# Kernel tuning notes

Measured on AMD Instinct MI355X. Metric: run time of the kernel, lower is better.

## Reference

```python
import jax, jax.numpy as jnp
import numpy as np

B, T, E, D = 8, 2048, 1024, 128


def setup_inputs() -> dict:
    key = jax.random.key(0)
    k1, k2, k3, k4 = jax.random.split(key, 4)
    x = jax.random.normal(k1, (B, T, E), dtype=jnp.float32)
    wq = jax.random.normal(k2, (E, D), dtype=jnp.float32) * (E ** -0.5)
    wk = jax.random.normal(k3, (E, D), dtype=jnp.float32) * (E ** -0.5)
    wv = jax.random.normal(k4, (E, D), dtype=jnp.float32) * (E ** -0.5)
    return {"x": x, "wq": wq, "wk": wk, "wv": wv}


def reference(x, wq, wk, wv):
    # Projections (bias-free Linear): [B,T,E] @ [E,D] -> [B,T,D]
    q = x @ wq
    k = x @ wk
    v = x @ wv
    d = k.shape[-1]
    # Faithful to source: scores / d**(-0.5) == scores * sqrt(d)
    scores = jnp.einsum('btd,bsd->bts', q, k) * (d ** 0.5)
    causal = jnp.tril(jnp.ones((x.shape[1], x.shape[1]), dtype=bool))
    scores = jnp.where(causal, scores, -jnp.inf)
    weights = jax.nn.softmax(scores, axis=-1)  # dropout omitted (eval mode)
    return jnp.einsum('bts,bsd->btd', weights, v)
```

## Files before the change

kernel.cpp:

```cpp
#include <hip/hip_runtime.h>


#define NB 8
#define NT 2048
#define NE 1024
#define ND 128

typedef unsigned short U16;
typedef unsigned int U32;
typedef __attribute__((ext_vector_type(8))) short vbf8;
typedef __attribute__((ext_vector_type(4))) float vf4;

#define EXP2F(x) __builtin_amdgcn_exp2f(x)

__device__ __forceinline__ U16 f2bf(float f) {
  U32 u = __builtin_bit_cast(U32, f);
  u += 0x7fffu + ((u >> 16) & 1u);
  return (U16)(u >> 16);
}
__device__ __forceinline__ float bf2f(U16 h) {
  U32 u = ((U32)h) << 16;
  return __builtin_bit_cast(float, u);
}
__device__ __forceinline__ void gl_lds16(const void* g, void* l) {
  __builtin_amdgcn_global_load_lds((__attribute__((address_space(1))) void*)g,
                                   (__attribute__((address_space(3))) void*)l, 16, 0, 0);
}

__global__ void wsplit_kernel(const float* __restrict__ wq, const float* __restrict__ wk,
                              const float* __restrict__ wv, U16* __restrict__ wth,
                              U16* __restrict__ wtl) {
  int id = blockIdx.x * 256 + threadIdx.x;
  if (id >= 384 * 1024) return;
  int n = id >> 10, e = id & 1023;
  float v;
  if (n < 128)      v = wq[e * 128 + n] * 16.322231701033217f;
  else if (n < 256) v = wk[e * 128 + (n - 128)];
  else              v = wv[e * 128 + (n - 256)];
  U16 h = f2bf(v);
  wth[id] = h;
  wtl[id] = f2bf(v - bf2f(h));
}

__global__ __launch_bounds__(256, 3) void qkv_kernel(
    const float* __restrict__ x, const U16* __restrict__ wth, const U16* __restrict__ wtl,
    U16* __restrict__ qfh, U16* __restrict__ qfl, U16* __restrict__ kfh,
    U16* __restrict__ kfl, U16* __restrict__ vf) {
  __shared__ __align__(16) char smem[49152];
  char* Ah = smem;
  char* Al = smem + 8192;
  char* Bh = smem + 16384;
  char* Bl = smem + 32768;

  const int tid = threadIdx.x;
  const int w = tid >> 6, lane = tid & 63;
  const int fr = lane & 15, fq = lane >> 4;
  const int m0 = blockIdx.x * 64;
  const int nt = blockIdx.y;
  const U16* bh_src = wth + nt * (128 * 1024);
  const U16* bl_src = wtl + nt * (128 * 1024);

  const vf4 vzero = {0.f, 0.f, 0.f, 0.f};
  vf4 acc[2][4];
#pragma unroll
  for (int i = 0; i < 2; ++i)
#pragma unroll
    for (int j = 0; j < 4; ++j) acc[i][j] = vzero;

  const int wm = (w >> 1) * 32, wn = (w & 1) * 64;
  const int arow = tid >> 2, ag = tid & 3;
  const float* abase = x + (size_t)(m0 + arow) * 1024 + ag * 8;

  float v0[8], v1[8];
  {
    const float* s = abase;
    ((float4*)v0)[0] = *(const float4*)(s);
    ((float4*)v0)[1] = *(const float4*)(s + 4);
    ((float4*)v1)[0] = *(const float4*)(s + 32);
    ((float4*)v1)[1] = *(const float4*)(s + 36);
  }

  for (int k0 = 0; k0 < 1024; k0 += 64) {
#pragma unroll
    for (int p = 0; p < 4; ++p) {
      const int g = p * 256 + tid;
      const int row = g >> 3, c = g & 7;
      const int sc = c ^ (row & 7);
      const int ldsb = (p * 256 + w * 64) * 16;
      gl_lds16(bh_src + row * 1024 + k0 + sc * 8, Bh + ldsb);
      if (nt < 2) gl_lds16(bl_src + row * 1024 + k0 + sc * 8, Bl + ldsb);
    }
    {
      vbf8 h0, l0, h1, l1;
#pragma unroll
      for (int i = 0; i < 8; ++i) {
        U16 a = f2bf(v0[i]);
        h0[i] = (short)a; l0[i] = (short)f2bf(v0[i] - bf2f(a));
        U16 b = f2bf(v1[i]);
        h1[i] = (short)b; l1[i] = (short)f2bf(v1[i] - bf2f(b));
      }
      const int sw = arow & 7;
      *(vbf8*)(Ah + arow * 128 + ((ag ^ sw) << 4))       = h0;
      *(vbf8*)(Ah + arow * 128 + (((ag + 4) ^ sw) << 4)) = h1;
      if (nt < 2) {
        *(vbf8*)(Al + arow * 128 + ((ag ^ sw) << 4))       = l0;
        *(vbf8*)(Al + arow * 128 + (((ag + 4) ^ sw) << 4)) = l1;
      }
    }
    __syncthreads();

    if (k0 + 64 < 1024) {
      const float* s = abase + k0 + 64;
      ((float4*)v0)[0] = *(const float4*)(s);
      ((float4*)v0)[1] = *(const float4*)(s + 4);
      ((float4*)v1)[0] = *(const float4*)(s + 32);
      ((float4*)v1)[1] = *(const float4*)(s + 36);
    }

    if (nt < 2) {
#pragma unroll
      for (int kc = 0; kc < 2; ++kc) {
        vbf8 a_h[2], a_l[2], b_h[4], b_l[4];
#pragma unroll
        for (int i = 0; i < 2; ++i) {
          const int row = wm + i * 16 + fr;
          const int off = row * 128 + (((kc * 4 + fq) ^ (row & 7)) << 4);
          a_h[i] = *(const vbf8*)(Ah + off);
          a_l[i] = *(const vbf8*)(Al + off);
        }
#pragma unroll
        for (int j = 0; j < 4; ++j) {
          const int row = wn + j * 16 + fr;
          const int off = row * 128 + (((kc * 4 + fq) ^ (row & 7)) << 4);
          b_h[j] = *(const vbf8*)(Bh + off);
          b_l[j] = *(const vbf8*)(Bl + off);
        }
#pragma unroll
        for (int i = 0; i < 2; ++i)
#pragma unroll
          for (int j = 0; j < 4; ++j) {
            acc[i][j] = __builtin_amdgcn_mfma_f32_16x16x32_bf16(a_h[i], b_h[j], acc[i][j], 0, 0, 0);
            acc[i][j] = __builtin_amdgcn_mfma_f32_16x16x32_bf16(a_h[i], b_l[j], acc[i][j], 0, 0, 0);
            acc[i][j] = __builtin_amdgcn_mfma_f32_16x16x32_bf16(a_l[i], b_h[j], acc[i][j], 0, 0, 0);
          }
      }
    } else {
#pragma unroll
      for (int kc = 0; kc < 2; ++kc) {
        vbf8 a_h[2], b_h[4];
#pragma unroll
        for (int i = 0; i < 2; ++i) {
          const int row = wm + i * 16 + fr;
          a_h[i] = *(const vbf8*)(Ah + row * 128 + (((kc * 4 + fq) ^ (row & 7)) << 4));
        }
#pragma unroll
        for (int j = 0; j < 4; ++j) {
          const int row = wn + j * 16 + fr;
          b_h[j] = *(const vbf8*)(Bh + row * 128 + (((kc * 4 + fq) ^ (row & 7)) << 4));
        }
#pragma unroll
        for (int i = 0; i < 2; ++i)
#pragma unroll
          for (int j = 0; j < 4; ++j)
            acc[i][j] = __builtin_amdgcn_mfma_f32_16x16x32_bf16(a_h[i], b_h[j], acc[i][j], 0, 0, 0);
      }
    }
    __syncthreads();
  }

  const int b = m0 >> 11;
  if (nt < 2) {
    U16* tlh = (U16*)smem;
    U16* tll = (U16*)(smem + 16896);
#pragma unroll
    for (int i = 0; i < 2; ++i)
#pragma unroll
      for (int j = 0; j < 4; ++j)
#pragma unroll
        for (int r = 0; r < 4; ++r) {
          const int ml = wm + i * 16 + fq * 4 + r;
          const int col = wn + j * 16 + fr;
          const float val = acc[i][j][r];
          const U16 h = f2bf(val);
          tlh[ml * 132 + col] = h;
          tll[ml * 132 + col] = f2bf(val - bf2f(h));
        }
    __syncthreads();
    U16* dh = (nt == 0) ? qfh : kfh;
    U16* dl = (nt == 0) ? qfl : kfl;
    const int g0 = (m0 & 2047) >> 4;
#pragma unroll
    for (int p = 0; p < 4; ++p) {
      const int idx = p * 256 + tid;
      const int gl = idx >> 8, kc = (idx >> 6) & 3, ln = idx & 63;
      const int row = gl * 16 + (ln & 15);
      const int colc = kc * 32 + (ln >> 4) * 8;
      const size_t o = (((size_t)b * 128 + g0 + gl) * 4 + kc) * 512 + ln * 8;
      *(vbf8*)(dh + o) = *(const vbf8*)(tlh + row * 132 + colc);
      *(vbf8*)(dl + o) = *(const vbf8*)(tll + row * 132 + colc);
    }
  } else {
    U16* tl = (U16*)smem;
#pragma unroll
    for (int i = 0; i < 2; ++i)
#pragma unroll
      for (int j = 0; j < 4; ++j)
#pragma unroll
        for (int r = 0; r < 4; ++r) {
          const int ml = wm + i * 16 + fq * 4 + r;
          const int col = wn + j * 16 + fr;
          tl[col * 68 + ml] = f2bf(acc[i][j][r]);
        }
    __syncthreads();
    const int sc0 = (m0 & 2047) >> 5;
#pragma unroll
    for (int p = 0; p < 4; ++p) {
      const int idx = p * 256 + tid;
      const int df = idx >> 7, sc = (idx >> 6) & 1, ln = idx & 63;
      const int d = df * 16 + (ln & 15);
      const int sl = sc * 32 + (ln >> 4) * 8;
      const size_t o = (((size_t)b * 8 + df) * 64 + (sc0 + sc)) * 512 + ln * 8;
      *(vbf8*)(vf + o) = *(const vbf8*)(tl + d * 68 + sl);
    }
  }
}

__global__ __launch_bounds__(256, 3) void flash_kernel(
    const U16* __restrict__ qfh, const U16* __restrict__ qfl,
    const U16* __restrict__ kfh, const U16* __restrict__ kfl,
    const U16* __restrict__ vf, float* __restrict__ out) {
  __shared__ __align__(16) char smem[25088];

  const int tid = threadIdx.x;
  const int w = tid >> 6, lane = tid & 63;
  const int fr = lane & 15, fq = lane >> 4;
  const int sq = w;
  const int bid = blockIdx.x;
  const int bb = bid & 7;
  const int jj = bid >> 3;
  const int g = (jj < 64) ? (127 - jj) : (jj - 64);
  const int q0g = g * 16;

  vbf8 q_h[4], q_l[4];
  {
    const U16* qb = qfh + ((size_t)bb * 128 + g) * 2048 + lane * 8;
    const U16* qlb = qfl + ((size_t)bb * 128 + g) * 2048 + lane * 8;
#pragma unroll
    for (int kc = 0; kc < 4; ++kc) {
      q_h[kc] = *(const vbf8*)(qb + kc * 512);
      q_l[kc] = *(const vbf8*)(qlb + kc * 512);
    }
  }

  const U16* khp = kfh + (size_t)bb * 262144 + (size_t)(sq * 4) * 2048 + lane * 8;
  const U16* klp = kfl + (size_t)bb * 262144 + (size_t)(sq * 4) * 2048 + lane * 8;
  const U16* vfp = vf + (size_t)bb * 262144 + (size_t)(sq * 2) * 512 + lane * 8;
  U16* pw = (U16*)(smem + w * 2304);

  const vf4 vzero = {0.f, 0.f, 0.f, 0.f};
  vf4 oacc[8];
#pragma unroll
  for (int i = 0; i < 8; ++i) oacc[i] = vzero;
  float m_r[4], l_r[4];
#pragma unroll
  for (int r = 0; r < 4; ++r) { m_r[r] = -__builtin_inff(); l_r[r] = 0.f; }

  const int lim = q0g + 15 - sq * 64;
  const int ntw = (lim >= 0) ? ((lim >> 8) + 1) : 0;

  for (int T = 0; T < ntw; ++T) {
    vf4 sacc[4] = {vzero, vzero, vzero, vzero};
    __builtin_amdgcn_s_setprio(1);
#pragma unroll
    for (int sf = 0; sf < 4; ++sf) {
#pragma unroll
      for (int kc = 0; kc < 4; ++kc) {
        const vbf8 kh_r = *(const vbf8*)(khp + sf * 2048 + kc * 512);
        const vbf8 kl_r = *(const vbf8*)(klp + sf * 2048 + kc * 512);
        sacc[sf] = __builtin_amdgcn_mfma_f32_16x16x32_bf16(q_h[kc], kh_r, sacc[sf], 0, 0, 0);
        sacc[sf] = __builtin_amdgcn_mfma_f32_16x16x32_bf16(q_h[kc], kl_r, sacc[sf], 0, 0, 0);
        sacc[sf] = __builtin_amdgcn_mfma_f32_16x16x32_bf16(q_l[kc], kh_r, sacc[sf], 0, 0, 0);
      }
    }
    __builtin_amdgcn_s_setprio(0);

    if (T == ntw - 1) {
#pragma unroll
      for (int sf = 0; sf < 4; ++sf) {
        const int s_g = T * 256 + sq * 64 + sf * 16 + fr;
#pragma unroll
        for (int r = 0; r < 4; ++r)
          if (s_g > q0g + fq * 4 + r) sacc[sf][r] = -__builtin_inff();
      }
    }

    float tmax[4];
#pragma unroll
    for (int r = 0; r < 4; ++r)
      tmax[r] = fmaxf(fmaxf(sacc[0][r], sacc[1][r]), fmaxf(sacc[2][r], sacc[3][r]));
#pragma unroll
    for (int off = 1; off < 16; off <<= 1)
#pragma unroll
      for (int r = 0; r < 4; ++r) tmax[r] = fmaxf(tmax[r], __shfl_xor(tmax[r], off, 64));

    vbf8 vreg[8][2];
#pragma unroll
    for (int df = 0; df < 8; ++df) {
      vreg[df][0] = *(const vbf8*)(vfp + df * 32768);
      vreg[df][1] = *(const vbf8*)(vfp + df * 32768 + 512);
    }

    bool need = false;
    float mne[4];
#pragma unroll
    for (int r = 0; r < 4; ++r) {
      need |= (tmax[r] > m_r[r]);
      const float mn = fmaxf(m_r[r], tmax[r]);
      mne[r] = (mn == -__builtin_inff()) ? 0.f : mn;
    }
    if (__any(need)) {
#pragma unroll
      for (int r = 0; r < 4; ++r) {
        const float alpha = EXP2F(m_r[r] - mne[r]);
        l_r[r] *= alpha;
        m_r[r] = fmaxf(m_r[r], tmax[r]);
#pragma unroll
        for (int i = 0; i < 8; ++i) oacc[i][r] *= alpha;
      }
    }

    float psum[4];
    U16 pb[4][4];
#pragma unroll
    for (int sf = 0; sf < 4; ++sf)
#pragma unroll
      for (int r = 0; r < 4; ++r) {
        const float pv = EXP2F(sacc[sf][r] - mne[r]);
        psum[r] = (sf == 0) ? pv : (psum[r] + pv);
        pb[sf][r] = f2bf(pv);
      }
#pragma unroll
    for (int off = 1; off < 16; off <<= 1)
#pragma unroll
      for (int r = 0; r < 4; ++r) psum[r] += __shfl_xor(psum[r], off, 64);
#pragma unroll
    for (int r = 0; r < 4; ++r) l_r[r] += psum[r];

#pragma unroll
    for (int sf = 0; sf < 4; ++sf)
#pragma unroll
      for (int r = 0; r < 4; ++r) pw[(fq * 4 + r) * 72 + sf * 16 + fr] = pb[sf][r];
    asm volatile("s_waitcnt lgkmcnt(0)" ::: "memory");
    const vbf8 pf0 = *(const vbf8*)(pw + fr * 72 + fq * 8);
    const vbf8 pf1 = *(const vbf8*)(pw + fr * 72 + 32 + fq * 8);

    __builtin_amdgcn_s_setprio(1);
#pragma unroll
    for (int df = 0; df < 8; ++df) {
      oacc[df] = __builtin_amdgcn_mfma_f32_16x16x32_bf16(pf0, vreg[df][0], oacc[df], 0, 0, 0);
      oacc[df] = __builtin_amdgcn_mfma_f32_16x16x32_bf16(pf1, vreg[df][1], oacc[df], 0, 0, 0);
    }
    __builtin_amdgcn_s_setprio(0);

    khp += 32768; klp += 32768; vfp += 4096;
  }

  __syncthreads();
  float* O_d = (float*)smem;
  float* m_s = (float*)(smem + 24576);
  float* l_s = (float*)(smem + 24832);
  if (sq > 0) {
#pragma unroll
    for (int i = 0; i < 8; ++i)
#pragma unroll
      for (int r = 0; r < 4; ++r)
        O_d[((sq - 1) * 16 + fq * 4 + r) * 128 + i * 16 + fr] = oacc[i][r];
  }
  if (fr == 0) {
#pragma unroll
    for (int r = 0; r < 4; ++r) {
      m_s[sq * 16 + fq * 4 + r] = m_r[r];
      l_s[sq * 16 + fq * 4 + r] = l_r[r];
    }
  }
  __syncthreads();
  if (sq == 0) {
#pragma unroll
    for (int r = 0; r < 4; ++r) {
      const int row = fq * 4 + r;
      float mv[4];
      float M = -__builtin_inff();
#pragma unroll
      for (int p = 0; p < 4; ++p) {
        mv[p] = m_s[p * 16 + row];
        M = fmaxf(M, mv[p]);
      }
      float wgt[4], denom = 0.f;
#pragma unroll
      for (int p = 0; p < 4; ++p) {
        wgt[p] = EXP2F(mv[p] - M);
        denom += wgt[p] * l_s[p * 16 + row];
      }
      const float inv = 1.f / denom;
#pragma unroll
      for (int i = 0; i < 8; ++i) {
        float o = wgt[0] * oacc[i][r];
#pragma unroll
        for (int p = 1; p < 4; ++p)
          o += wgt[p] * O_d[((p - 1) * 16 + row) * 128 + i * 16 + fr];
        out[(size_t)(bb * 2048 + q0g + row) * 128 + i * 16 + fr] = o * inv;
      }
    }
  }
}

extern "C" void kernel_launch(void* const* d_in, const int* in_sizes, int n_in, void* d_out,
                              int out_size, void* d_ws, size_t ws_size, hipStream_t stream) {
  const float* x = (const float*)d_in[0];
  const float* wq = (const float*)d_in[1];
  const float* wk = (const float*)d_in[2];
  const float* wv = (const float*)d_in[3];
  char* ws = (char*)d_ws;
  U16* wth = (U16*)(ws);
  U16* wtl = (U16*)(ws + 786432);
  U16* qfh = (U16*)(ws + 1572864);
  U16* qfl = (U16*)(ws + 5767168);
  U16* kfh = (U16*)(ws + 9961472);
  U16* kfl = (U16*)(ws + 14155776);
  U16* vfr = (U16*)(ws + 18350080);
  float* out = (float*)d_out;

  wsplit_kernel<<<dim3(1536), dim3(256), 0, stream>>>(wq, wk, wv, wth, wtl);
  qkv_kernel<<<dim3(256, 3), dim3(256), 0, stream>>>(x, wth, wtl, qfh, qfl, kfh, kfl, vfr);
  flash_kernel<<<dim3(1024), dim3(256), 0, stream>>>(qfh, qfl, kfh, kfl, vfr, out);
}
```

Before: 94.45 us.

## Split flash attention KV loop across two blocks and merge partials

Each query tile's KV iterations are split between two blocks that take alternating 256-key chunks. Each block writes an unnormalized partial output along with its row max and row sum to workspace, and a new merge kernel combines the two halves. The goal is to double the grid size and shorten the longest causal tiles, which improves load balance and occupancy. The cost is an extra kernel launch plus partial-output traffic (about 17 MB written and read back). The split path is used only when the workspace is large enough, and a guard handles rows whose max is -inf.

```diff
diff --git a/kernel.cpp b/kernel.cpp
--- a/kernel.cpp
+++ b/kernel.cpp
@@ -225,17 +225,20 @@
   }
 }
 
-__global__ __launch_bounds__(256, 3) void flash_kernel(
+template <int SPLIT>
+__global__ __launch_bounds__(256, 3) void flash_kernel_t(
     const U16* __restrict__ qfh, const U16* __restrict__ qfl,
     const U16* __restrict__ kfh, const U16* __restrict__ kfl,
-    const U16* __restrict__ vf, float* __restrict__ out) {
+    const U16* __restrict__ vf, float* __restrict__ out, float* __restrict__ part) {
   __shared__ __align__(16) char smem[25088];
 
   const int tid = threadIdx.x;
   const int w = tid >> 6, lane = tid & 63;
   const int fr = lane & 15, fq = lane >> 4;
   const int sq = w;
-  const int bid = blockIdx.x;
+  const int bid2 = blockIdx.x;
+  const int half = SPLIT ? (bid2 & 1) : 0;
+  const int bid = SPLIT ? (bid2 >> 1) : bid2;
   const int bb = bid & 7;
   const int jj = bid >> 3;
   const int g = (jj < 64) ? (127 - jj) : (jj - 64);
@@ -252,9 +255,12 @@
     }
   }
 
-  const U16* khp = kfh + (size_t)bb * 262144 + (size_t)(sq * 4) * 2048 + lane * 8;
-  const U16* klp = kfl + (size_t)bb * 262144 + (size_t)(sq * 4) * 2048 + lane * 8;
-  const U16* vfp = vf + (size_t)bb * 262144 + (size_t)(sq * 2) * 512 + lane * 8;
+  const U16* khp = kfh + (size_t)bb * 262144 + (size_t)(sq * 4) * 2048 + lane * 8
+                   + (size_t)half * 32768;
+  const U16* klp = kfl + (size_t)bb * 262144 + (size_t)(sq * 4) * 2048 + lane * 8
+                   + (size_t)half * 32768;
+  const U16* vfp = vf + (size_t)bb * 262144 + (size_t)(sq * 2) * 512 + lane * 8
+                   + (size_t)half * 4096;
   U16* pw = (U16*)(smem + w * 2304);
 
   const vf4 vzero = {0.f, 0.f, 0.f, 0.f};
@@ -267,8 +273,11 @@
 
   const int lim = q0g + 15 - sq * 64;
   const int ntw = (lim >= 0) ? ((lim >> 8) + 1) : 0;
-
-  for (int T = 0; T < ntw; ++T) {
+  const int my_n = SPLIT ? ((ntw > half) ? ((ntw - half + 1) >> 1) : 0) : ntw;
+  const int tstep = SPLIT ? 2 : 1;
+
+  for (int it = 0; it < my_n; ++it) {
+    const int T = half + it * tstep;
     vf4 sacc[4] = {vzero, vzero, vzero, vzero};
     __builtin_amdgcn_s_setprio(1);
 #pragma unroll
@@ -362,7 +371,7 @@
     }
     __builtin_amdgcn_s_setprio(0);
 
-    khp += 32768; klp += 32768; vfp += 4096;
+    khp += 32768 * tstep; klp += 32768 * tstep; vfp += 4096 * tstep;
   }
 
   __syncthreads();
@@ -385,6 +394,7 @@
   }
   __syncthreads();
   if (sq == 0) {
+    float* pO = SPLIT ? (part + ((size_t)(bb * 128 + g) * 2 + half) * 2112) : (float*)0;
 #pragma unroll
     for (int r = 0; r < 4; ++r) {
       const int row = fq * 4 + r;
@@ -395,23 +405,60 @@
         mv[p] = m_s[p * 16 + row];
         M = fmaxf(M, mv[p]);
       }
+      const float Mne = (M == -__builtin_inff()) ? 0.f : M;
       float wgt[4], denom = 0.f;
 #pragma unroll
       for (int p = 0; p < 4; ++p) {
-        wgt[p] = EXP2F(mv[p] - M);
+        wgt[p] = EXP2F(mv[p] - Mne);
         denom += wgt[p] * l_s[p * 16 + row];
       }
-      const float inv = 1.f / denom;
-#pragma unroll
-      for (int i = 0; i < 8; ++i) {
-        float o = wgt[0] * oacc[i][r];
-#pragma unroll
-        for (int p = 1; p < 4; ++p)
-          o += wgt[p] * O_d[((p - 1) * 16 + row) * 128 + i * 16 + fr];
-        out[(size_t)(bb * 2048 + q0g + row) * 128 + i * 16 + fr] = o * inv;
-      }
-    }
-  }
+      if (SPLIT) {
+#pragma unroll
+        for (int i = 0; i < 8; ++i) {
+          float o = wgt[0] * oacc[i][r];
+#pragma unroll
+          for (int p = 1; p < 4; ++p)
+            o += wgt[p] * O_d[((p - 1) * 16 + row) * 128 + i * 16 + fr];
+          pO[row * 128 + i * 16 + fr] = o;
+        }
+        if (fr == 0) {
+          pO[2048 + row] = M;
+          pO[2064 + row] = denom;
+        }
+      } else {
+        const float inv = 1.f / denom;
+#pragma unroll
+        for (int i = 0; i < 8; ++i) {
+          float o = wgt[0] * oacc[i][r];
+#pragma unroll
+          for (int p = 1; p < 4; ++p)
+            o += wgt[p] * O_d[((p - 1) * 16 + row) * 128 + i * 16 + fr];
+          out[(size_t)(bb * 2048 + q0g + row) * 128 + i * 16 + fr] = o * inv;
+        }
+      }
+    }
+  }
+}
+
+__global__ __launch_bounds__(256) void fmerge_kernel(const float* __restrict__ part,
+                                                     float* __restrict__ out) {
+  const int tid = threadIdx.x;
+  const int rg = blockIdx.x * 16 + (tid >> 4);
+  const int c8 = (tid & 15) * 8;
+  const int b = rg >> 11, rb = rg & 2047, g = rb >> 4, r16 = rb & 15;
+  const float* p0 = part + ((size_t)(b * 128 + g) * 2 + 0) * 2112;
+  const float* p1 = part + ((size_t)(b * 128 + g) * 2 + 1) * 2112;
+  const float M0 = p0[2048 + r16], M1 = p1[2048 + r16];
+  const float L0 = p0[2064 + r16], L1 = p1[2064 + r16];
+  const float M = fmaxf(M0, M1);
+  const float e0 = EXP2F(M0 - M);
+  const float e1 = EXP2F(M1 - M);
+  const float inv = 1.f / (L0 * e0 + L1 * e1);
+  const float* a0 = p0 + r16 * 128 + c8;
+  const float* a1 = p1 + r16 * 128 + c8;
+  float* o = out + (size_t)rg * 128 + c8;
+#pragma unroll
+  for (int j = 0; j < 8; ++j) o[j] = (a0[j] * e0 + a1[j] * e1) * inv;
 }
 
 extern "C" void kernel_launch(void* const* d_in, const int* in_sizes, int n_in, void* d_out,
@@ -428,9 +475,17 @@
   U16* kfh = (U16*)(ws + 9961472);
   U16* kfl = (U16*)(ws + 14155776);
   U16* vfr = (U16*)(ws + 18350080);
+  float* part = (float*)(ws + 22544384);
   float* out = (float*)d_out;
 
   wsplit_kernel<<<dim3(1536), dim3(256), 0, stream>>>(wq, wk, wv, wth, wtl);
   qkv_kernel<<<dim3(256, 3), dim3(256), 0, stream>>>(x, wth, wtl, qfh, qfl, kfh, kfl, vfr);
-  flash_kernel<<<dim3(1024), dim3(256), 0, stream>>>(qfh, qfl, kfh, kfl, vfr, out);
-}
+
+  const size_t need = 22544384ull + 2048ull * 2112ull * 4ull;
+  if (ws_size >= need) {
+    flash_kernel_t<1><<<dim3(2048), dim3(256), 0, stream>>>(qfh, qfl, kfh, kfl, vfr, out, part);
+    fmerge_kernel<<<dim3(1024), dim3(256), 0, stream>>>(part, out);
+  } else {
+    flash_kernel_t<0><<<dim3(1024), dim3(256), 0, stream>>>(qfh, qfl, kfh, kfl, vfr, out, part);
+  }
+}
```

Result: slower. 120.3 us (+27.4%).
